# Performance work log

Hardware: AMD Instinct MI355X
Metric: run time of the kernel (lower is better)

Reference implementation:

```python
import jax, jax.numpy as jnp
import numpy as np

D_MODEL = 1024
NUM_HEADS = 16
DEPTH = D_MODEL // NUM_HEADS


def setup_inputs() -> dict:
    key = jax.random.key(0)
    ks = jax.random.split(key, 11)
    B, S, D = 2, 2048, D_MODEL
    s = 1.0 / np.sqrt(D)
    inp = {
        'x': jax.random.normal(ks[0], (B, S, D), jnp.float32),
        'pH': jax.random.normal(ks[1], (B, 1, 1), jnp.float32),
        'Wq': jax.random.normal(ks[2], (D, D), jnp.float32) * s,
        'bq': jnp.zeros((D,), jnp.float32),
        'Wk': jax.random.normal(ks[3], (D, D), jnp.float32) * s,
        'bk': jnp.zeros((D,), jnp.float32),
        'Wv': jax.random.normal(ks[4], (D, D), jnp.float32) * s,
        'bv': jnp.zeros((D,), jnp.float32),
        'Wo': jax.random.normal(ks[5], (D, D), jnp.float32) * s,
        'bo': jnp.zeros((D,), jnp.float32),
    }
    return inp


def reference(x, pH, Wq, bq, Wk, bk, Wv, bv, Wo, bo):
    B, S, D = x.shape
    H, dh = NUM_HEADS, DEPTH
    # QKV projections -> [B, H, S, dh]
    def proj(W, b):
        return (x @ W + b).reshape(B, S, H, dh).transpose(0, 2, 1, 3)
    q = proj(Wq, bq)
    k = proj(Wk, bk)
    v = proj(Wv, bv)
    # scores [B, H, S, S] with additive per-sample pH bias broadcast over heads/positions
    scores = jnp.einsum('bhqd,bhkd->bhqk', q, k) / jnp.sqrt(jnp.asarray(dh, x.dtype))
    scores = scores + pH[:, :, :, None]  # [B,1,1,1] broadcasts to [B,H,S,S]
    attn = jax.nn.softmax(scores, axis=-1)
    out = jnp.einsum('bhqk,bhkd->bhqd', attn, v)  # [B,H,S,dh]
    out = out.transpose(0, 2, 1, 3).reshape(B, S, D)
    return out @ Wo + bo  # dropout p=0.0 -> identity
```

## Files before the change

kernel.cpp:

```cpp
#include <hip/hip_runtime.h>
#include <hip/hip_bf16.h>
#include <math.h>

#define BATCH 2
#define SEQ   2048
#define DMODEL 1024
#define NHEADS 16
#define DHEAD 64
#define MROWS (BATCH*SEQ)

typedef __attribute__((ext_vector_type(8))) short bf16x8;
typedef __attribute__((ext_vector_type(4))) short bf16x4;
typedef __attribute__((ext_vector_type(4))) float f32x4;

__device__ __forceinline__ short f2bf(float f) {
    union { float f; unsigned u; } c; c.f = f;
    unsigned r = (c.u + 0x7fffu + ((c.u >> 16) & 1u)) >> 16;
    return (short)r;
}

__device__ __forceinline__ void async_ld16(const void* g, void* l) {
    __builtin_amdgcn_global_load_lds(
        (const __attribute__((address_space(1))) unsigned*)g,
        (__attribute__((address_space(3))) unsigned*)l, 16, 0, 0);
}

__global__ __launch_bounds__(256) void convert_h(
    const float* __restrict__ in, short* __restrict__ hi, int n8)
{
    const int i = blockIdx.x * 256 + threadIdx.x;
    if (i >= n8) return;
    const float4* p = (const float4*)in + (size_t)i * 2;
    float4 a = p[0], b = p[1];
    float v[8] = {a.x, a.y, a.z, a.w, b.x, b.y, b.z, b.w};
    bf16x8 H;
    #pragma unroll
    for (int j = 0; j < 8; ++j) H[j] = f2bf(v[j]);
    *((bf16x8*)hi + i) = H;
}

__global__ __launch_bounds__(256) void transpose_w4(
    const float* __restrict__ W0, const float* __restrict__ W1,
    const float* __restrict__ W2, const float* __restrict__ W3,
    short* __restrict__ oqkv, short* __restrict__ oo)
{
    __shared__ float T[64][65];
    const int tid = threadIdx.x;
    const int z = blockIdx.z;
    const float* W = (z == 0) ? W0 : (z == 1) ? W1 : (z == 2) ? W2 : W3;
    short* out = (z < 3) ? (oqkv + (size_t)z * 1024 * 1024) : oo;
    const int n0 = blockIdx.x * 64, k0 = blockIdx.y * 64;
    #pragma unroll
    for (int i = 0; i < 16; ++i) {
        const int idx = tid + i * 256;
        const int r = idx >> 6, c = idx & 63;
        T[r][c] = W[(size_t)(k0 + r) * DMODEL + n0 + c];
    }
    __syncthreads();
    #pragma unroll
    for (int i = 0; i < 4; ++i) {
        const int idx = tid + i * 256;
        const int r = idx >> 4, g = idx & 15;
        bf16x4 H;
        #pragma unroll
        for (int j = 0; j < 4; ++j)
            H[j] = f2bf(T[g * 4 + j][r]);
        *(bf16x4*)(out + (size_t)(n0 + r) * DMODEL + k0 + g * 4) = H;
    }
}

#define GBK 64

__global__ __launch_bounds__(256) void mfma_gemm(
    const short* __restrict__ Ahi, const short* __restrict__ Bthi,
    const float* __restrict__ b0, const float* __restrict__ b1, const float* __restrict__ b2,
    short* __restrict__ oqh, short* __restrict__ okh, short* __restrict__ ovh,
    float* __restrict__ outf, int mode, float qscale)
{
    __shared__ short Ah[128 * GBK], Bh[128 * GBK];

    const int tid  = threadIdx.x;
    const int lane = tid & 63;
    const int w    = tid >> 6;
    const int quad = lane >> 4;
    const int l15  = lane & 15;
    const int wr   = w >> 1, wc = w & 1;
    const int m0   = blockIdx.y * 128;
    const int n0   = blockIdx.x * 128;
    const int K    = DMODEL;

    f32x4 acc[4][4] = {};

    int srow[4], spos[4];
    #pragma unroll
    for (int j = 0; j < 4; ++j) {
        const int c = w * 256 + j * 64 + lane;
        srow[j] = c >> 3;
        spos[j] = (c & 7) ^ (srow[j] & 7);
    }

    for (int k0 = 0; k0 < K; k0 += GBK) {
        __syncthreads();
        #pragma unroll
        for (int j = 0; j < 4; ++j) {
            const int cB = (w * 256 + j * 64) * 8;
            async_ld16(Ahi + (size_t)(m0 + srow[j]) * K + k0 + spos[j] * 8, Ah + cB);
            async_ld16(Bthi + (size_t)(n0 + srow[j]) * K + k0 + spos[j] * 8, Bh + cB);
        }
        __syncthreads();

        #pragma unroll
        for (int s = 0; s < 2; ++s) {
            bf16x8 afh[4], bfh[4];
            #pragma unroll
            for (int mi = 0; mi < 4; ++mi) {
                const int row = wr * 64 + mi * 16 + l15;
                const int pos = (s * 4 + quad) ^ (row & 7);
                afh[mi] = *(const bf16x8*)(Ah + row * GBK + pos * 8);
            }
            #pragma unroll
            for (int ni = 0; ni < 4; ++ni) {
                const int row = wc * 64 + ni * 16 + l15;
                const int pos = (s * 4 + quad) ^ (row & 7);
                bfh[ni] = *(const bf16x8*)(Bh + row * GBK + pos * 8);
            }
            #pragma unroll
            for (int mi = 0; mi < 4; ++mi)
                #pragma unroll
                for (int ni = 0; ni < 4; ++ni)
                    acc[mi][ni] = __builtin_amdgcn_mfma_f32_16x16x32_bf16(
                        afh[mi], bfh[ni], acc[mi][ni], 0, 0, 0);
        }
    }

    const int nbase = n0 + wc * 64;
    if (mode == 1) {
        #pragma unroll
        for (int mi = 0; mi < 4; ++mi)
            #pragma unroll
            for (int ni = 0; ni < 4; ++ni)
                #pragma unroll
                for (int r = 0; r < 4; ++r) {
                    const int m = m0 + wr * 64 + mi * 16 + quad * 4 + r;
                    const int nn = nbase + ni * 16 + l15;
                    outf[(size_t)m * DMODEL + nn] = acc[mi][ni][r] + b0[nn];
                }
    } else {
        __syncthreads();
        short* scr = (w < 2) ? (Ah + w * 4096) : (Bh + (w - 2) * 4096);
        const int which = nbase >> 10;
        const int hh = (nbase & 1023) >> 6;
        const int mb = m0 + wr * 64;
        const int b = mb >> 11, sbase = mb & (SEQ - 1);

        if (which < 2) {
            const float* bias = which ? b1 : b0;
            short* dstp = which ? okh : oqh;
            const float scl = which ? 1.0f : qscale;
            #pragma unroll
            for (int mi = 0; mi < 4; ++mi)
                #pragma unroll
                for (int ni = 0; ni < 4; ++ni)
                    #pragma unroll
                    for (int r = 0; r < 4; ++r) {
                        const int sloc = mi * 16 + quad * 4 + r;
                        const int dloc = ni * 16 + l15;
                        const int nn = (nbase + ni * 16 + l15) & 1023;
                        scr[sloc * 64 + (((dloc >> 3) ^ (sloc & 7)) * 8) + (dloc & 7)] =
                            f2bf((acc[mi][ni][r] + bias[nn]) * scl);
                    }
            #pragma unroll
            for (int i = 0; i < 8; ++i) {
                const int sloc = i * 8 + (lane >> 3);
                const int cph = (lane & 7) ^ (sloc & 7);
                bf16x8 row = *(const bf16x8*)(scr + sloc * 64 + cph * 8);
                const int dloc = (lane & 7) * 8;
                *(bf16x8*)(dstp + ((size_t)(b * NHEADS + hh) * SEQ + sbase + sloc) * DHEAD + dloc) = row;
            }
        } else {
            #pragma unroll
            for (int mi = 0; mi < 4; ++mi)
                #pragma unroll
                for (int ni = 0; ni < 4; ++ni)
                    #pragma unroll
                    for (int r = 0; r < 4; ++r) {
                        const int sloc = mi * 16 + quad * 4 + r;
                        const int dloc = ni * 16 + l15;
                        const int nn = (nbase + ni * 16 + l15) & 1023;
                        scr[dloc * 64 + (((sloc >> 3) ^ (dloc & 7)) * 8) + (sloc & 7)] =
                            f2bf(acc[mi][ni][r] + b2[nn]);
                    }
            #pragma unroll
            for (int i = 0; i < 8; ++i) {
                const int dloc = i * 8 + (lane >> 3);
                const int cph = (lane & 7) ^ (dloc & 7);
                bf16x8 row = *(const bf16x8*)(scr + dloc * 64 + cph * 8);
                const int sg = sbase + (lane & 7) * 8;
                *(bf16x8*)(ovh + ((size_t)(b * NHEADS + hh) * DHEAD + dloc) * SEQ + sg) = row;
            }
        }
    }
}

#define PP 72

__global__ __launch_bounds__(256) void attn_mfma(
    const short* __restrict__ Qh_g, const short* __restrict__ Kh_g,
    const short* __restrict__ Vth_g, short* __restrict__ Oh_g)
{
    __shared__ short Ksh[2][4096];
    __shared__ short Vsh[2][4096];
    __shared__ short Ph[4][2][16 * PP];

    const int tid  = threadIdx.x;
    const int lane = tid & 63;
    const int w    = tid >> 6;
    const int quad = lane >> 4;
    const int l15  = lane & 15;

    const int bh    = blockIdx.x & 31;
    const int qtile = blockIdx.x >> 5;
    const int q0    = qtile * 128 + w * 32;
    const size_t kvb = (size_t)bh * SEQ * DHEAD;

    bf16x8 ones;
    #pragma unroll
    for (int j = 0; j < 8; ++j) ones[j] = (short)0x3f80;

    bf16x8 qA[2], qB[2];
    {
        const size_t qrA = kvb + (size_t)(q0 + l15) * DHEAD;
        const size_t qrB = kvb + (size_t)(q0 + 16 + l15) * DHEAD;
        qA[0] = *(const bf16x8*)(Qh_g + qrA + quad * 8);
        qA[1] = *(const bf16x8*)(Qh_g + qrA + 32 + quad * 8);
        qB[0] = *(const bf16x8*)(Qh_g + qrB + quad * 8);
        qB[1] = *(const bf16x8*)(Qh_g + qrB + 32 + quad * 8);
    }

    const bool isv = (w >= 2);
    int srow[4], spos[4];
    #pragma unroll
    for (int j = 0; j < 4; ++j) {
        const int c = (w & 1) * 256 + j * 64 + lane;
        srow[j] = c >> 3;
        spos[j] = (c & 7) ^ (srow[j] & 7);
    }

    auto stage = [&](int buf, int kb) {
        short* d = isv ? Vsh[buf] : Ksh[buf];
        const short* src = isv ? (Vth_g + kvb + kb) : (Kh_g + kvb + (size_t)kb * DHEAD);
        #pragma unroll
        for (int j = 0; j < 4; ++j) {
            const short* g = src + (isv ? ((size_t)srow[j] * SEQ + spos[j] * 8)
                                        : ((size_t)srow[j] * DHEAD + spos[j] * 8));
            async_ld16(g, d + ((w & 1) * 256 + j * 64) * 8);
        }
    };

    f32x4 oA[4] = {}, oB[4] = {};
    f32x4 lAv = {}, lBv = {};

    stage(0, 0);
    int pb = 0;
    for (int kb = 0; kb < SEQ; kb += 64, pb ^= 1) {
        __syncthreads();
        if (kb + 64 < SEQ) stage(pb ^ 1, kb + 64);

        const short* Kb = Ksh[pb];
        const short* Vb = Vsh[pb];

        #pragma unroll
        for (int mf = 0; mf < 4; ++mf) {
            const int row = mf * 16 + l15;
            const int sw = row & 7;
            bf16x8 kh0 = *(const bf16x8*)(Kb + row * 64 + ((quad ^ sw) * 8));
            bf16x8 kh1 = *(const bf16x8*)(Kb + row * 64 + (((4 + quad) ^ sw) * 8));
            f32x4 cA = {}, cB = {};
            cA = __builtin_amdgcn_mfma_f32_16x16x32_bf16(kh0, qA[0], cA, 0, 0, 0);
            cA = __builtin_amdgcn_mfma_f32_16x16x32_bf16(kh1, qA[1], cA, 0, 0, 0);
            cB = __builtin_amdgcn_mfma_f32_16x16x32_bf16(kh0, qB[0], cB, 0, 0, 0);
            cB = __builtin_amdgcn_mfma_f32_16x16x32_bf16(kh1, qB[1], cB, 0, 0, 0);

            unsigned uA[4], uB[4];
            #pragma unroll
            for (int r = 0; r < 4; ++r) {
                union { float f; unsigned u; } p;
                p.f = __builtin_amdgcn_exp2f(cA[r]);
                uA[r] = p.u;
                p.f = __builtin_amdgcn_exp2f(cB[r]);
                uB[r] = p.u;
            }
            uint2 pkA, pkB;
            pkA.x = __builtin_amdgcn_perm(uA[1], uA[0], 0x07060302u);
            pkA.y = __builtin_amdgcn_perm(uA[3], uA[2], 0x07060302u);
            pkB.x = __builtin_amdgcn_perm(uB[1], uB[0], 0x07060302u);
            pkB.y = __builtin_amdgcn_perm(uB[3], uB[2], 0x07060302u);
            *(uint2*)(&Ph[w][0][l15 * PP + mf * 16 + quad * 4]) = pkA;
            *(uint2*)(&Ph[w][1][l15 * PP + mf * 16 + quad * 4]) = pkB;
        }

        bf16x8 pA0 = *(const bf16x8*)(&Ph[w][0][l15 * PP + quad * 8]);
        bf16x8 pA1 = *(const bf16x8*)(&Ph[w][0][l15 * PP + 32 + quad * 8]);
        bf16x8 pB0 = *(const bf16x8*)(&Ph[w][1][l15 * PP + quad * 8]);
        bf16x8 pB1 = *(const bf16x8*)(&Ph[w][1][l15 * PP + 32 + quad * 8]);

        lAv = __builtin_amdgcn_mfma_f32_16x16x32_bf16(pA0, ones, lAv, 0, 0, 0);
        lAv = __builtin_amdgcn_mfma_f32_16x16x32_bf16(pA1, ones, lAv, 0, 0, 0);
        lBv = __builtin_amdgcn_mfma_f32_16x16x32_bf16(pB0, ones, lBv, 0, 0, 0);
        lBv = __builtin_amdgcn_mfma_f32_16x16x32_bf16(pB1, ones, lBv, 0, 0, 0);

        #pragma unroll
        for (int nf = 0; nf < 4; ++nf) {
            const int row = nf * 16 + l15;
            const int sw = row & 7;
            bf16x8 vh0 = *(const bf16x8*)(Vb + row * 64 + ((quad ^ sw) * 8));
            bf16x8 vh1 = *(const bf16x8*)(Vb + row * 64 + (((4 + quad) ^ sw) * 8));
            f32x4 cA = oA[nf], cB = oB[nf];
            cA = __builtin_amdgcn_mfma_f32_16x16x32_bf16(pA0, vh0, cA, 0, 0, 0);
            cA = __builtin_amdgcn_mfma_f32_16x16x32_bf16(pA1, vh1, cA, 0, 0, 0);
            cB = __builtin_amdgcn_mfma_f32_16x16x32_bf16(pB0, vh0, cB, 0, 0, 0);
            cB = __builtin_amdgcn_mfma_f32_16x16x32_bf16(pB1, vh1, cB, 0, 0, 0);
            oA[nf] = cA; oB[nf] = cB;
        }
    }

    float liA[4], liB[4];
    #pragma unroll
    for (int r = 0; r < 4; ++r) {
        liA[r] = 1.0f / lAv[r];
        liB[r] = 1.0f / lBv[r];
    }

    const int b = bh >> 4, hh = bh & 15;
    #pragma unroll
    for (int nf = 0; nf < 4; ++nf) {
        #pragma unroll
        for (int r = 0; r < 4; ++r) {
            const int qa = q0 + quad * 4 + r;
            const int d = nf * 16 + l15;
            Oh_g[(size_t)(b * SEQ + qa) * DMODEL + hh * DHEAD + d] = f2bf(oA[nf][r] * liA[r]);
            Oh_g[(size_t)(b * SEQ + qa + 16) * DMODEL + hh * DHEAD + d] = f2bf(oB[nf][r] * liB[r]);
        }
    }
}

extern "C" void kernel_launch(void* const* d_in, const int* in_sizes, int n_in,
                              void* d_out, int out_size, void* d_ws, size_t ws_size,
                              hipStream_t stream) {
    const float* x  = (const float*)d_in[0];
    const float* Wq = (const float*)d_in[2];
    const float* bq = (const float*)d_in[3];
    const float* Wk = (const float*)d_in[4];
    const float* bk = (const float*)d_in[5];
    const float* Wv = (const float*)d_in[6];
    const float* bv = (const float*)d_in[7];
    const float* Wo = (const float*)d_in[8];
    const float* bo = (const float*)d_in[9];
    float* out = (float*)d_out;

    char* ws = (char*)d_ws;
    const size_t MB = 1024 * 1024;
    short* qh  = (short*)(ws + 0 * MB);
    short* kh  = (short*)(ws + 16 * MB);
    short* vth = (short*)(ws + 32 * MB);
    short* aoh = (short*)(ws + 48 * MB);
    short* xhi = (short*)(ws + 64 * MB);
    short* wqkv_hi = (short*)(ws + 80 * MB);
    short* wto_hi  = (short*)(ws + 92 * MB);

    dim3 blk(256);
    const int n8 = MROWS * DMODEL / 8;

    hipLaunchKernelGGL(convert_h, dim3(n8 / 256), blk, 0, stream, x, xhi, n8);
    hipLaunchKernelGGL(transpose_w4, dim3(16, 16, 4), blk, 0, stream,
                       Wq, Wk, Wv, Wo, wqkv_hi, wto_hi);

    const float qscale = 0.125f * 1.44269504088896f;
    hipLaunchKernelGGL(mfma_gemm, dim3(3072 / 128, MROWS / 128), blk, 0, stream,
                       xhi, wqkv_hi, bq, bk, bv,
                       qh, kh, vth, (float*)nullptr, 0, qscale);

    hipLaunchKernelGGL(attn_mfma, dim3(BATCH * NHEADS * (SEQ / 128)), blk, 0, stream,
                       qh, kh, vth, aoh);

    hipLaunchKernelGGL(mfma_gemm, dim3(1024 / 128, MROWS / 128), blk, 0, stream,
                       aoh, wto_hi, bo, bo, bo,
                       (short*)nullptr, (short*)nullptr, (short*)nullptr,
                       out, 1, 1.0f);
}
```

Before: 208.8 us.

## Split attention along KV into two halves and combine partials; fuse prep kernels

The attention kernel now splits the key/value sequence into two halves, doubling the grid from 512 to 1024 blocks. Each half writes unnormalized fp32 partial outputs and row sums, and a new combine kernel adds them, normalizes, and converts to bf16. This is meant to improve occupancy and load balance across the GPU's CUs. It costs extra fp32 traffic (two 16MB partial buffers) and one more launch. The x conversion and weight transpose are also merged into one prep kernel to save a launch. The combine skips max-rescaling, which relies on the scores having no running-max subtraction, the same as the original kernel.

```diff
diff --git a/kernel.cpp b/kernel.cpp
--- a/kernel.cpp
+++ b/kernel.cpp
@@ -25,31 +25,31 @@
         (__attribute__((address_space(3))) unsigned*)l, 16, 0, 0);
 }
 
-__global__ __launch_bounds__(256) void convert_h(
-    const float* __restrict__ in, short* __restrict__ hi, int n8)
-{
-    const int i = blockIdx.x * 256 + threadIdx.x;
-    if (i >= n8) return;
-    const float4* p = (const float4*)in + (size_t)i * 2;
-    float4 a = p[0], b = p[1];
-    float v[8] = {a.x, a.y, a.z, a.w, b.x, b.y, b.z, b.w};
-    bf16x8 H;
-    #pragma unroll
-    for (int j = 0; j < 8; ++j) H[j] = f2bf(v[j]);
-    *((bf16x8*)hi + i) = H;
-}
-
-__global__ __launch_bounds__(256) void transpose_w4(
+__global__ __launch_bounds__(256) void prep(
+    const float* __restrict__ x, short* __restrict__ xhi,
     const float* __restrict__ W0, const float* __restrict__ W1,
     const float* __restrict__ W2, const float* __restrict__ W3,
     short* __restrict__ oqkv, short* __restrict__ oo)
 {
     __shared__ float T[64][65];
     const int tid = threadIdx.x;
-    const int z = blockIdx.z;
+    if (blockIdx.x < 2048) {
+        const int i = blockIdx.x * 256 + tid;
+        const float4* p = (const float4*)x + (size_t)i * 2;
+        float4 a = p[0], b = p[1];
+        float v[8] = {a.x, a.y, a.z, a.w, b.x, b.y, b.z, b.w};
+        bf16x8 H;
+        #pragma unroll
+        for (int j = 0; j < 8; ++j) H[j] = f2bf(v[j]);
+        *((bf16x8*)xhi + i) = H;
+        return;
+    }
+    const int bi = blockIdx.x - 2048;
+    const int z = bi >> 8;
+    const int t = bi & 255;
     const float* W = (z == 0) ? W0 : (z == 1) ? W1 : (z == 2) ? W2 : W3;
     short* out = (z < 3) ? (oqkv + (size_t)z * 1024 * 1024) : oo;
-    const int n0 = blockIdx.x * 64, k0 = blockIdx.y * 64;
+    const int n0 = (t & 15) * 64, k0 = (t >> 4) * 64;
     #pragma unroll
     for (int i = 0; i < 16; ++i) {
         const int idx = tid + i * 256;
@@ -206,7 +206,9 @@
 
 __global__ __launch_bounds__(256) void attn_mfma(
     const short* __restrict__ Qh_g, const short* __restrict__ Kh_g,
-    const short* __restrict__ Vth_g, short* __restrict__ Oh_g)
+    const short* __restrict__ Vth_g,
+    float* __restrict__ op0, float* __restrict__ op1,
+    float* __restrict__ l0g, float* __restrict__ l1g)
 {
     __shared__ short Ksh[2][4096];
     __shared__ short Vsh[2][4096];
@@ -219,7 +221,8 @@
     const int l15  = lane & 15;
 
     const int bh    = blockIdx.x & 31;
-    const int qtile = blockIdx.x >> 5;
+    const int sk    = (blockIdx.x >> 5) & 1;
+    const int qtile = blockIdx.x >> 6;
     const int q0    = qtile * 128 + w * 32;
     const size_t kvb = (size_t)bh * SEQ * DHEAD;
 
@@ -260,11 +263,12 @@
     f32x4 oA[4] = {}, oB[4] = {};
     f32x4 lAv = {}, lBv = {};
 
-    stage(0, 0);
+    const int kb0 = sk * (SEQ / 2), kb1 = kb0 + SEQ / 2;
+    stage(0, kb0);
     int pb = 0;
-    for (int kb = 0; kb < SEQ; kb += 64, pb ^= 1) {
+    for (int kb = kb0; kb < kb1; kb += 64, pb ^= 1) {
         __syncthreads();
-        if (kb + 64 < SEQ) stage(pb ^ 1, kb + 64);
+        if (kb + 64 < kb1) stage(pb ^ 1, kb + 64);
 
         const short* Kb = Ksh[pb];
         const short* Vb = Vsh[pb];
@@ -324,24 +328,57 @@
         }
     }
 
-    float liA[4], liB[4];
+    float* op = sk ? op1 : op0;
+    float* lg = sk ? l1g : l0g;
+    const int b = bh >> 4, hh = bh & 15;
     #pragma unroll
     for (int r = 0; r < 4; ++r) {
-        liA[r] = 1.0f / lAv[r];
-        liB[r] = 1.0f / lBv[r];
-    }
-
-    const int b = bh >> 4, hh = bh & 15;
+        const int qa = q0 + quad * 4 + r;
+        if (l15 == 0) {
+            lg[bh * SEQ + qa] = lAv[r];
+            lg[bh * SEQ + qa + 16] = lBv[r];
+        }
+    }
     #pragma unroll
     for (int nf = 0; nf < 4; ++nf) {
         #pragma unroll
         for (int r = 0; r < 4; ++r) {
             const int qa = q0 + quad * 4 + r;
             const int d = nf * 16 + l15;
-            Oh_g[(size_t)(b * SEQ + qa) * DMODEL + hh * DHEAD + d] = f2bf(oA[nf][r] * liA[r]);
-            Oh_g[(size_t)(b * SEQ + qa + 16) * DMODEL + hh * DHEAD + d] = f2bf(oB[nf][r] * liB[r]);
-        }
-    }
+            op[(size_t)(b * SEQ + qa) * DMODEL + hh * DHEAD + d] = oA[nf][r];
+            op[(size_t)(b * SEQ + qa + 16) * DMODEL + hh * DHEAD + d] = oB[nf][r];
+        }
+    }
+}
+
+__global__ __launch_bounds__(256) void combine_o(
+    const float* __restrict__ op0, const float* __restrict__ op1,
+    const float* __restrict__ l0g, const float* __restrict__ l1g,
+    short* __restrict__ aoh)
+{
+    const int i = blockIdx.x * 256 + threadIdx.x;
+    const size_t e = (size_t)i * 8;
+    const int qg = (int)(e >> 10);
+    const int col = (int)(e & 1023);
+    const int b = qg >> 11;
+    const int q = qg & (SEQ - 1);
+    const int bh = b * NHEADS + (col >> 6);
+    const float inv = 1.0f / (l0g[bh * SEQ + q] + l1g[bh * SEQ + q]);
+
+    float4 a0 = *(const float4*)(op0 + e);
+    float4 a1 = *(const float4*)(op0 + e + 4);
+    float4 c0 = *(const float4*)(op1 + e);
+    float4 c1 = *(const float4*)(op1 + e + 4);
+    bf16x8 H;
+    H[0] = f2bf((a0.x + c0.x) * inv);
+    H[1] = f2bf((a0.y + c0.y) * inv);
+    H[2] = f2bf((a0.z + c0.z) * inv);
+    H[3] = f2bf((a0.w + c0.w) * inv);
+    H[4] = f2bf((a1.x + c1.x) * inv);
+    H[5] = f2bf((a1.y + c1.y) * inv);
+    H[6] = f2bf((a1.z + c1.z) * inv);
+    H[7] = f2bf((a1.w + c1.w) * inv);
+    *((bf16x8*)aoh + i) = H;
 }
 
 extern "C" void kernel_launch(void* const* d_in, const int* in_sizes, int n_in,
@@ -364,24 +401,29 @@
     short* kh  = (short*)(ws + 16 * MB);
     short* vth = (short*)(ws + 32 * MB);
     short* aoh = (short*)(ws + 48 * MB);
+    float* op0 = (float*)(ws + 56 * MB);
     short* xhi = (short*)(ws + 64 * MB);
+    float* op1 = (float*)(ws + 72 * MB);
     short* wqkv_hi = (short*)(ws + 80 * MB);
+    float* l0g = (float*)(ws + 88 * MB);
+    float* l1g = (float*)(ws + 89 * MB);
     short* wto_hi  = (short*)(ws + 92 * MB);
 
     dim3 blk(256);
-    const int n8 = MROWS * DMODEL / 8;
-
-    hipLaunchKernelGGL(convert_h, dim3(n8 / 256), blk, 0, stream, x, xhi, n8);
-    hipLaunchKernelGGL(transpose_w4, dim3(16, 16, 4), blk, 0, stream,
-                       Wq, Wk, Wv, Wo, wqkv_hi, wto_hi);
+
+    hipLaunchKernelGGL(prep, dim3(2048 + 1024), blk, 0, stream,
+                       x, xhi, Wq, Wk, Wv, Wo, wqkv_hi, wto_hi);
 
     const float qscale = 0.125f * 1.44269504088896f;
     hipLaunchKernelGGL(mfma_gemm, dim3(3072 / 128, MROWS / 128), blk, 0, stream,
                        xhi, wqkv_hi, bq, bk, bv,
                        qh, kh, vth, (float*)nullptr, 0, qscale);
 
-    hipLaunchKernelGGL(attn_mfma, dim3(BATCH * NHEADS * (SEQ / 128)), blk, 0, stream,
-                       qh, kh, vth, aoh);
+    hipLaunchKernelGGL(attn_mfma, dim3(BATCH * NHEADS * (SEQ / 128) * 2), blk, 0, stream,
+                       qh, kh, vth, op0, op1, l0g, l1g);
+
+    hipLaunchKernelGGL(combine_o, dim3(MROWS * DMODEL / 8 / 256), blk, 0, stream,
+                       op0, op1, l0g, l1g, aoh);
 
     hipLaunchKernelGGL(mfma_gemm, dim3(1024 / 128, MROWS / 128), blk, 0, stream,
                        aoh, wto_hi, bo, bo, bo,
```

New measurement: 213.9 us. 2.5% more time.
